# Kernel tuning notes

Hardware: AMD Instinct MI355X
Metric: run time of the kernel (lower is better)

The kernel has to match this reference:

```python
import jax, jax.numpy as jnp
import numpy as np

EPS = 1e-5
NEG_SLOPE = 0.2

def _bn(h, gamma, beta, axes):
    # training-mode batch norm (batch statistics), matching torch BN forward in train mode
    mu = jnp.mean(h, axis=axes, keepdims=True)
    var = jnp.var(h, axis=axes, keepdims=True)
    return (h - mu) * jax.lax.rsqrt(var + EPS) * gamma + beta

def _lrelu(h):
    return jnp.where(h >= 0, h, NEG_SLOPE * h)

def _edge_conv(x, idx, W, gamma, beta):
    # x: (B,N,C) channels-last; idx: (B,N,k) neighbor indices into N
    # gathered[b,n,j,c] = x[b, idx[b,n,j], c]
    gathered = jnp.take_along_axis(x[:, None, :, :], idx[:, :, :, None], axis=2)  # (B,N,k,C)
    xc = jnp.broadcast_to(x[:, :, None, :], gathered.shape)
    feat = jnp.concatenate([gathered - xc, xc], axis=-1)          # (B,N,k,2C)
    h = jnp.einsum('bnkc,oc->bnko', feat, W)                       # 1x1 conv
    h = _lrelu(_bn(h, gamma, beta, axes=(0, 1, 2)))
    return jnp.max(h, axis=2)                                      # max over k -> (B,N,O)

def setup_inputs() -> dict:
    key = jax.random.key(0)
    ks = jax.random.split(key, 20)
    B, N, K = 8, 2048, 20
    d = {
        'x': jax.random.normal(ks[0], (B, 3, N), jnp.float32),
        'geod_dist': jax.random.normal(ks[1], (B, N, N), jnp.float32),
        'W1': jax.random.normal(ks[2], (64, 6), jnp.float32) * 0.1,
        'g1': jnp.ones((64,)), 'bt1': jnp.zeros((64,)),
        'W2': jax.random.normal(ks[3], (64, 128), jnp.float32) * 0.1,
        'g2': jnp.ones((64,)), 'bt2': jnp.zeros((64,)),
        'W3': jax.random.normal(ks[4], (128, 128), jnp.float32) * 0.1,
        'g3': jnp.ones((128,)), 'bt3': jnp.zeros((128,)),
        'W4': jax.random.normal(ks[5], (256, 256), jnp.float32) * 0.1,
        'g4': jnp.ones((256,)), 'bt4': jnp.zeros((256,)),
        'W5': jax.random.normal(ks[6], (1024, 512), jnp.float32) * 0.05,
        'g5': jnp.ones((1024,)), 'bt5': jnp.zeros((1024,)),
        'L1': jax.random.normal(ks[7], (512, 2048), jnp.float32) * 0.02,
        'g6': jnp.ones((512,)), 'bt6': jnp.zeros((512,)),
        'L2': jax.random.normal(ks[8], (256, 512), jnp.float32) * 0.05,
        'bl2': jnp.zeros((256,)),
        'g7': jnp.ones((256,)), 'bt7': jnp.zeros((256,)),
        'L3': jax.random.normal(ks[9], (40, 256), jnp.float32) * 0.05,
        'bl3': jnp.zeros((40,)),
    }
    return d

def reference(x, geod_dist, W1, g1, bt1, W2, g2, bt2, W3, g3, bt3, W4, g4, bt4,
              W5, g5, bt5, L1, g6, bt6, L2, bl2, g7, bt7, L3, bl3):
    K = 20
    # neighbor indices from geodesic distance (topk largest, as in source)
    idx = jax.lax.top_k(geod_dist, K)[1]            # (B,N,K)
    xt = jnp.transpose(x, (0, 2, 1))                # (B,N,3)
    x1 = _edge_conv(xt, idx, W1, g1, bt1)           # (B,N,64)
    x2 = _edge_conv(x1, idx, W2, g2, bt2)           # (B,N,64)
    x3 = _edge_conv(x2, idx, W3, g3, bt3)           # (B,N,128)
    x4 = _edge_conv(x3, idx, W4, g4, bt4)           # (B,N,256)
    cat = jnp.concatenate([x1, x2, x3, x4], axis=-1)  # (B,N,512)
    h = jnp.einsum('bnc,oc->bno', cat, W5)            # 1x1 conv1d -> (B,N,1024)
    h = _lrelu(_bn(h, g5, bt5, axes=(0, 1)))
    hmax = jnp.max(h, axis=1)                        # (B,1024)
    havg = jnp.mean(h, axis=1)                       # (B,1024)
    z = jnp.concatenate([hmax, havg], axis=1)        # (B,2048)
    z = _lrelu(_bn(z @ L1.T, g6, bt6, axes=(0,)))    # (B,512)
    z = _lrelu(_bn(z @ L2.T + bl2, g7, bt7, axes=(0,)))  # (B,256); dropout = identity (eval)
    return z @ L3.T + bl3                            # (B,40)
```

## Files before the change

### kernel.cpp

```cpp
#include <hip/hip_runtime.h>
#include <hip/hip_bf16.h>
#include <cstdint>
#include <cstddef>

#define NB 8
#define NP 2048
#define NK 20
#define BN 16384

typedef _Float16 half8 __attribute__((ext_vector_type(8)));
typedef _Float16 half4v __attribute__((ext_vector_type(4)));
typedef float f32x4 __attribute__((ext_vector_type(4)));

__device__ __forceinline__ void gload_lds16(const void* g, void* l) {
  __builtin_amdgcn_global_load_lds(
      (const __attribute__((address_space(1))) unsigned int*)g,
      (__attribute__((address_space(3))) unsigned int*)l, 16, 0, 0);
}

static constexpr size_t OFF_IDX   = 0;
static constexpr size_t OFF_XT    = OFF_IDX + (size_t)BN*NK*4;
static constexpr size_t OFF_XCATH = OFF_XT + (size_t)BN*3*4;
static constexpr size_t OFF_WT1   = OFF_XCATH + (size_t)BN*512*2;
static constexpr size_t OFF_WD1   = OFF_WT1 + 3*64*4;
static constexpr size_t OFF_BC2   = OFF_WD1 + 3*64*4;
static constexpr size_t OFF_BC3   = OFF_BC2 + (size_t)64*128*2;
static constexpr size_t OFF_BC4   = OFF_BC3 + (size_t)64*256*2;
static constexpr size_t OFF_B5    = OFF_BC4 + (size_t)128*512*2;
static constexpr size_t OFF_YH    = OFF_B5 + (size_t)512*1024*2;
static constexpr size_t OFF_HMAX  = OFF_YH + (size_t)BN*512*2;
static constexpr size_t OFF_HMIN  = OFF_HMAX + (size_t)BN*256*4;
static constexpr size_t OFF_H5    = OFF_HMAX;
static constexpr size_t OFF_PART  = OFF_HMIN + (size_t)BN*256*4;
static constexpr size_t OFF_PMEAN = OFF_PART + (size_t)8*1024*1024;
static constexpr size_t OFF_SS    = OFF_PMEAN + (size_t)8*8*1024*4;
static constexpr size_t OFF_Z     = OFF_SS + 2*1024*4;
static constexpr size_t OFF_Z1P   = OFF_Z + (size_t)NB*2048*4;
static constexpr size_t OFF_Z1    = OFF_Z1P + NB*512*4;
static constexpr size_t OFF_Z2P   = OFF_Z1 + NB*512*4;
static constexpr size_t OFF_Z2    = OFF_Z2P + NB*256*4;

__device__ __forceinline__ void prep_b_dev(const float* __restrict__ W,
                                           _Float16* __restrict__ Bp, int t,
                                           int K2, int lgO, int lgRS) {
  int O = 1 << lgO;
  int o = t & (O - 1), k = t >> lgO;
  float v = W[((size_t)o << lgRS) + k];
  int ch = k >> 6, ks = (k >> 5) & 1, kg = (k >> 3) & 3, e = k & 7;
  int sl = o >> 4, ol = o & 15;
  size_t flat = (((size_t)(ch * 2 + ks) * (O >> 4) + sl) * 64 + (kg * 16 + ol)) * 8 + e;
  Bp[flat] = (_Float16)v;
}

__device__ __forceinline__ void prep_bc_dev(const float* __restrict__ W,
                                            _Float16* __restrict__ Bp, int t,
                                            int C, int lgO2, int lgRS) {
  int O2 = 1 << lgO2, O = O2 >> 1;
  int o2 = t & (O2 - 1), k = t >> lgO2;
  float v;
  if (o2 < O) v = W[((size_t)o2 << lgRS) + k];
  else {
    int o = o2 - O;
    v = W[((size_t)o << lgRS) + C + k] - W[((size_t)o << lgRS) + k];
  }
  int ch = k >> 6, ks = (k >> 5) & 1, kg = (k >> 3) & 3, e = k & 7;
  int sl = o2 >> 4, ol = o2 & 15;
  size_t flat = (((size_t)(ch * 2 + ks) * (O2 >> 4) + sl) * 64 + (kg * 16 + ol)) * 8 + e;
  Bp[flat] = (_Float16)v;
}

static constexpr int PB_TR  = 0;
static constexpr int PB_W1  = PB_TR + 192;
static constexpr int PB_BC2 = PB_W1 + 1;
static constexpr int PB_BC3 = PB_BC2 + 32;
static constexpr int PB_BC4 = PB_BC3 + 64;
static constexpr int PB_B5  = PB_BC4 + 256;
static constexpr int PB_END = PB_B5 + 2048;

__global__ __launch_bounds__(256) void k_prep_all(
    const float* __restrict__ x, float* __restrict__ xt,
    const float* __restrict__ W1, float* __restrict__ wt1, float* __restrict__ wd1,
    const float* __restrict__ W2, _Float16* __restrict__ bc2,
    const float* __restrict__ W3, _Float16* __restrict__ bc3,
    const float* __restrict__ W4, _Float16* __restrict__ bc4,
    const float* __restrict__ W5, _Float16* __restrict__ b5) {
  int blk = blockIdx.x, tid = threadIdx.x;
  if (blk < PB_W1) {
    int t = blk * 256 + tid;
    int n = t & (NP - 1);
    int c = (t / NP) % 3;
    int b = t / (3 * NP);
    xt[(size_t)(b * NP + n) * 3 + c] = x[t];
  } else if (blk < PB_BC2) {
    int t = tid;
    if (t < 192) {
      int o = t & 63, c = t >> 6;
      float w0 = W1[o * 6 + c];
      float w1 = W1[o * 6 + 3 + c];
      wt1[c * 64 + o] = w0;
      wd1[c * 64 + o] = w1 - w0;
    }
  } else if (blk < PB_BC3) prep_bc_dev(W2, bc2, (blk - PB_BC2) * 256 + tid, 64, 7, 7);
  else if (blk < PB_BC4)   prep_bc_dev(W3, bc3, (blk - PB_BC3) * 256 + tid, 64, 8, 7);
  else if (blk < PB_B5)    prep_bc_dev(W4, bc4, (blk - PB_BC4) * 256 + tid, 128, 9, 8);
  else                     prep_b_dev(W5, b5,   (blk - PB_B5) * 256 + tid, 512, 10, 9);
}

template <int CTRL>
__device__ __forceinline__ float dppmax(float x) {
  int t = __builtin_amdgcn_update_dpp(__float_as_int(x), __float_as_int(x),
                                      CTRL, 0xF, 0xF, false);
  return fmaxf(x, __int_as_float(t));
}
template <int CTRL>
__device__ __forceinline__ int dppmin(int x) {
  int t = __builtin_amdgcn_update_dpp(x, x, CTRL, 0xF, 0xF, false);
  return (t < x) ? t : x;
}
__device__ __forceinline__ float wave_max63(float x) {
  x = dppmax<0x111>(x); x = dppmax<0x112>(x); x = dppmax<0x114>(x);
  x = dppmax<0x118>(x); x = dppmax<0x142>(x); x = dppmax<0x143>(x);
  return x;
}
__device__ __forceinline__ int wave_min63(int x) {
  x = dppmin<0x111>(x); x = dppmin<0x112>(x); x = dppmin<0x114>(x);
  x = dppmin<0x118>(x); x = dppmin<0x142>(x); x = dppmin<0x143>(x);
  return x;
}

#define INS3(val, gi, m1, i1, m2, i2, m3, i3)            \
  {                                                      \
    bool c1 = (val) > m1;                                \
    float t_ = c1 ? m1 : (val); int ti_ = c1 ? i1 : (gi);\
    m1 = c1 ? (val) : m1;       i1 = c1 ? (gi) : i1;     \
    bool c2 = t_ > m2;                                   \
    float t2_ = c2 ? m2 : t_;   int t2i_ = c2 ? i2 : ti_;\
    m2 = c2 ? t_ : m2;          i2 = c2 ? ti_ : i2;      \
    bool c3 = t2_ > m3;                                  \
    m3 = c3 ? t2_ : m3;         i3 = c3 ? t2i_ : i3;     \
  }

#define SCAN3(v, m1, i1, m2, i2, m3, i3)                               \
  _Pragma("unroll")                                                    \
  for (int r = 0; r < 8; ++r) {                                        \
    float vals[4] = {v[r].x, v[r].y, v[r].z, v[r].w};                  \
    _Pragma("unroll")                                                  \
    for (int e = 0; e < 4; ++e) {                                      \
      float val = vals[e];                                             \
      int gi = r * 256 + l * 4 + e;                                    \
      INS3(val, gi, m1, i1, m2, i2, m3, i3)                            \
    }                                                                  \
  }

#define SCAN3M(v, dead, m1, i1, m2, i2, m3, i3)                        \
  _Pragma("unroll")                                                    \
  for (int r = 0; r < 8; ++r) {                                        \
    float vals[4] = {v[r].x, v[r].y, v[r].z, v[r].w};                  \
    _Pragma("unroll")                                                  \
    for (int e = 0; e < 4; ++e) {                                      \
      int el = r * 4 + e;                                              \
      float val = ((dead >> el) & 1u) ? NEG : vals[e];                 \
      int gi = r * 256 + l * 4 + e;                                    \
      INS3(val, gi, m1, i1, m2, i2, m3, i3)                            \
    }                                                                  \
  }

__global__ __launch_bounds__(256) void k_topk(const float* __restrict__ geod,
                                              int* __restrict__ idx) {
  int wv = threadIdx.x >> 6, l = threadIdx.x & 63;
  int row = blockIdx.x * 4 + wv;
  const float* g = geod + (size_t)row * NP;
  float4 v[8];
#pragma unroll
  for (int r = 0; r < 8; ++r) v[r] = *(const float4*)&g[r * 256 + l * 4];
  const float NEG = -__builtin_huge_valf();
  unsigned int dead = 0;
  float m1 = NEG, m2 = NEG, m3 = NEG;
  int i1 = 0, i2 = 0, i3 = 0;
  SCAN3(v, m1, i1, m2, i2, m3, i3)
  for (int it = 0; it < NK; ++it) {
    float xr = wave_max63(m1);
    float cv = __int_as_float(__builtin_amdgcn_readlane(__float_as_int(xr), 63));
    int ci = (m1 == cv) ? i1 : (1 << 30);
    ci = wave_min63(ci);
    int best_i = __builtin_amdgcn_readlane(ci, 63);
    if (l == 0) idx[(size_t)row * NK + it] = best_i;
    if (((best_i >> 2) & 63) == l) {
      dead |= 1u << (((best_i >> 8) << 2) | (best_i & 3));
      m1 = m2; i1 = i2; m2 = m3; i2 = i3; m3 = NEG; i3 = 0;
      if (m1 == NEG) { SCAN3M(v, dead, m1, i1, m2, i2, m3, i3) }
    }
  }
}

__global__ __launch_bounds__(256) void k_edge1(
    const float* __restrict__ xt, const int* __restrict__ idx,
    const float* __restrict__ wt1, const float* __restrict__ wd1,
    float* __restrict__ hmax, float* __restrict__ hmin,
    float* __restrict__ part) {
  __shared__ float xl[NP * 3];
  __shared__ int lidx[32 * NK];
  __shared__ float red[256];
  int tid = threadIdx.x;
  int b = blockIdx.x >> 6;
  int grp = blockIdx.x & 63;
  int p0 = grp * 32;
  for (int u = tid; u < NP * 3; u += 256) xl[u] = xt[(size_t)b * NP * 3 + u];
  for (int u = tid; u < 32 * NK; u += 256) lidx[u] = idx[((size_t)b * NP + p0) * NK + u];
  __syncthreads();
  int o = tid & 63;
  int pb = tid >> 6;
  float w0 = wt1[o], w1 = wt1[64 + o], w2 = wt1[128 + o];
  float d0 = wd1[o], d1 = wd1[64 + o], d2 = wd1[128 + o];
  float ps = 0.f, ps2 = 0.f;
#pragma unroll
  for (int i = 0; i < 8; ++i) {
    int pp = pb * 8 + i;
    int p = p0 + pp;
    float base = xl[p * 3] * d0 + xl[p * 3 + 1] * d1 + xl[p * 3 + 2] * d2;
    float mx = -3.4e38f, mn = 3.4e38f;
    for (int j = 0; j < NK; ++j) {
      int nb = lidx[pp * NK + j];
      float h = base + xl[nb * 3] * w0 + xl[nb * 3 + 1] * w1 + xl[nb * 3 + 2] * w2;
      mx = fmaxf(mx, h); mn = fminf(mn, h);
      ps += h; ps2 += h * h;
    }
    size_t P = (size_t)b * NP + p;
    hmax[P * 64 + o] = mx;
    hmin[P * 64 + o] = mn;
  }
  red[tid] = ps;
  __syncthreads();
  if (tid < 64) {
    float a = red[tid] + red[64 + tid] + red[128 + tid] + red[192 + tid];
    part[(size_t)blockIdx.x * 64 + tid] = a;
  }
  __syncthreads();
  red[tid] = ps2;
  __syncthreads();
  if (tid < 64) {
    float a = red[tid] + red[64 + tid] + red[128 + tid] + red[192 + tid];
    part[((size_t)gridDim.x + blockIdx.x) * 64 + tid] = a;
  }
}

template <int C, int O2, int NSPLIT>
__global__ __launch_bounds__(256) void k_dense_mfma(
    const _Float16* __restrict__ xh, int in_off,
    const _Float16* __restrict__ Bp, _Float16* __restrict__ yH) {
  constexpr int NCH = C / 64;
  constexpr int NO = O2 / NSPLIT;
  constexpr int NSLO = NO / 16;
  constexpr int NS = NSLO / 2;
  constexpr int PAIRS = 2 * NSLO;
  __shared__ __align__(16) _Float16 ldsA[64 * 64];
  __shared__ __align__(16) _Float16 ldsB[PAIRS * 512];
  int tid = threadIdx.x, wv = tid >> 6, l = tid & 63;
  int mblk = blockIdx.x, nid = 0;
  if (NSPLIT > 1) { nid = mblk >> 8; mblk &= 255; }
  int m0 = mblk * 64;
  int n_base = nid * NO;
  int mg = wv & 1, ng = wv >> 1;
  f32x4 acc[2][NS];
#pragma unroll
  for (int m = 0; m < 2; ++m)
#pragma unroll
    for (int s = 0; s < NS; ++s)
#pragma unroll
      for (int r = 0; r < 4; ++r) acc[m][s][r] = 0.f;

  for (int ch = 0; ch < NCH; ++ch) {
#pragma unroll
    for (int it = 0; it < 2; ++it) {
      int r0 = wv * 16 + it * 8;
      int R = r0 + (l >> 3);
      int q = (l & 7) ^ (l >> 3);
      gload_lds16(xh + (size_t)(m0 + R) * 512 + in_off + ch * 64 + q * 8, ldsA + r0 * 64);
    }
    for (int u = wv; u < PAIRS; u += 4) {
      int ks = u / NSLO, sloc = u - ks * NSLO;
      gload_lds16(Bp + ((size_t)((ch * 2 + ks) * (O2 / 16) + (n_base >> 4) + sloc) * 64 + l) * 8,
                  ldsB + u * 512);
    }
    __syncthreads();
#pragma unroll
    for (int ks = 0; ks < 2; ++ks) {
      half8 b[NS];
#pragma unroll
      for (int s = 0; s < NS; ++s)
        b[s] = *(const half8*)(ldsB + (ks * NSLO + ng * NS + s) * 512 + l * 8);
#pragma unroll
      for (int mt = 0; mt < 2; ++mt) {
        int row = mg * 32 + mt * 16 + (l & 15);
        int slot = (ks * 4 + (l >> 4)) ^ (row & 7);
        half8 a = *(const half8*)(ldsA + row * 64 + slot * 8);
#pragma unroll
        for (int s = 0; s < NS; ++s)
          acc[mt][s] = __builtin_amdgcn_mfma_f32_16x16x32_f16(a, b[s], acc[mt][s], 0, 0, 0);
      }
    }
    __syncthreads();
  }
  int g = l >> 4;
#pragma unroll
  for (int s = 0; s < NS; ++s) {
    int col = n_base + ng * (NS * 16) + s * 16 + (l & 15);
#pragma unroll
    for (int mt = 0; mt < 2; ++mt)
#pragma unroll
      for (int r = 0; r < 4; ++r) {
        int row = m0 + mg * 32 + mt * 16 + 4 * g + r;
        yH[(size_t)row * O2 + col] = (_Float16)acc[mt][s][r];
      }
  }
}

template <int O>
__global__ __launch_bounds__(256) void k_gather(
    const _Float16* __restrict__ yH, const int* __restrict__ idx,
    float* __restrict__ hmax, float* __restrict__ hmin,
    float* __restrict__ part) {
  constexpr int O2 = 2 * O;
  constexpr int CG = O / 4;
  constexpr int PPB = 256 / CG;
  __shared__ int lidx[PPB * NK];
  __shared__ float4 redS[256], redQ[256];
  int tid = threadIdx.x;
  int p0 = blockIdx.x * PPB;
  int bbase = p0 & ~(NP - 1);
  for (int u = tid; u < PPB * NK; u += 256) lidx[u] = idx[(size_t)p0 * NK + u];
  __syncthreads();
  int pp = tid / CG, g = tid - pp * CG;
  int p = p0 + pp;
  half4v sb4 = *(const half4v*)&yH[(size_t)p * O2 + O + g * 4];
  float sb[4] = {(float)sb4[0], (float)sb4[1], (float)sb4[2], (float)sb4[3]};
  float mx[4], mn[4], sm[4], sq[4];
#pragma unroll
  for (int e = 0; e < 4; ++e) { mx[e] = -3.4e38f; mn[e] = 3.4e38f; sm[e] = 0.f; sq[e] = 0.f; }
#pragma unroll
  for (int j = 0; j < NK; ++j) {
    int nb = bbase + lidx[pp * NK + j];
    half4v y4 = *(const half4v*)&yH[(size_t)nb * O2 + g * 4];
#pragma unroll
    for (int e = 0; e < 4; ++e) {
      float h = (float)y4[e] + sb[e];
      mx[e] = fmaxf(mx[e], h); mn[e] = fminf(mn[e], h);
      sm[e] += h; sq[e] += h * h;
    }
  }
  *(float4*)&hmax[(size_t)p * O + g * 4] = make_float4(mx[0], mx[1], mx[2], mx[3]);
  *(float4*)&hmin[(size_t)p * O + g * 4] = make_float4(mn[0], mn[1], mn[2], mn[3]);
  redS[tid] = make_float4(sm[0], sm[1], sm[2], sm[3]);
  redQ[tid] = make_float4(sq[0], sq[1], sq[2], sq[3]);
  __syncthreads();
  if (tid < CG) {
    float4 a = redS[tid], q = redQ[tid];
    for (int k = 1; k < PPB; ++k) {
      float4 b = redS[tid + k * CG], c = redQ[tid + k * CG];
      a.x += b.x; a.y += b.y; a.z += b.z; a.w += b.w;
      q.x += c.x; q.y += c.y; q.z += c.z; q.w += c.w;
    }
    *(float4*)&part[(size_t)blockIdx.x * O + tid * 4] = a;
    *(float4*)&part[((size_t)gridDim.x + blockIdx.x) * O + tid * 4] = q;
  }
}

__global__ __launch_bounds__(256) void k_conv5_mfma(
    const _Float16* __restrict__ xh, const _Float16* __restrict__ Bp,
    _Float16* __restrict__ h5, float* __restrict__ part) {
  __shared__ __align__(16) _Float16 ldsA[64 * 64];
  __shared__ __align__(16) _Float16 ldsB[32 * 512];
  __shared__ float ldsS[2][256], ldsQ[2][256], ldsMx[2][256], ldsMn[2][256];
  int tid = threadIdx.x, wv = tid >> 6, l = tid & 63;
  int mblk = blockIdx.x & 255, nid = blockIdx.x >> 8;
  int m0 = mblk * 64;
  int n_base = nid * 256;
  int mg = wv & 1, ng = wv >> 1;
  f32x4 acc[2][8];
#pragma unroll
  for (int m = 0; m < 2; ++m)
#pragma unroll
    for (int s = 0; s < 8; ++s)
#pragma unroll
      for (int r = 0; r < 4; ++r) acc[m][s][r] = 0.f;

  for (int ch = 0; ch < 8; ++ch) {
#pragma unroll
    for (int it = 0; it < 2; ++it) {
      int r0 = wv * 16 + it * 8;
      int R = r0 + (l >> 3);
      int q = (l & 7) ^ (l >> 3);
      gload_lds16(xh + (size_t)(m0 + R) * 512 + ch * 64 + q * 8, ldsA + r0 * 64);
    }
    for (int u = wv; u < 32; u += 4) {
      int ks = u >> 4, sloc = u & 15;
      gload_lds16(Bp + ((size_t)((ch * 2 + ks) * 64 + (n_base >> 4) + sloc) * 64 + l) * 8,
                  ldsB + u * 512);
    }
    __syncthreads();
#pragma unroll
    for (int ks = 0; ks < 2; ++ks) {
      half8 b[8];
#pragma unroll
      for (int s = 0; s < 8; ++s)
        b[s] = *(const half8*)(ldsB + (ks * 16 + ng * 8 + s) * 512 + l * 8);
#pragma unroll
      for (int mt = 0; mt < 2; ++mt) {
        int row = mg * 32 + mt * 16 + (l & 15);
        int slot = (ks * 4 + (l >> 4)) ^ (row & 7);
        half8 a = *(const half8*)(ldsA + row * 64 + slot * 8);
#pragma unroll
        for (int s = 0; s < 8; ++s)
          acc[mt][s] = __builtin_amdgcn_mfma_f32_16x16x32_f16(a, b[s], acc[mt][s], 0, 0, 0);
      }
    }
    __syncthreads();
  }
  int g = l >> 4;
#pragma unroll
  for (int s = 0; s < 8; ++s) {
    float sm = 0.f, sq = 0.f, mx = -3.4e38f, mn = 3.4e38f;
    int col = n_base + ng * 128 + s * 16 + (l & 15);
#pragma unroll
    for (int mt = 0; mt < 2; ++mt)
#pragma unroll
      for (int r = 0; r < 4; ++r) {
        float v = acc[mt][s][r];
        int row = m0 + mg * 32 + mt * 16 + 4 * g + r;
        h5[(size_t)row * 1024 + col] = (_Float16)v;
        sm += v; sq += v * v; mx = fmaxf(mx, v); mn = fminf(mn, v);
      }
    sm += __shfl_xor(sm, 16); sm += __shfl_xor(sm, 32);
    sq += __shfl_xor(sq, 16); sq += __shfl_xor(sq, 32);
    mx = fmaxf(mx, __shfl_xor(mx, 16)); mx = fmaxf(mx, __shfl_xor(mx, 32));
    mn = fminf(mn, __shfl_xor(mn, 16)); mn = fminf(mn, __shfl_xor(mn, 32));
    if (l < 16) {
      int u = ng * 128 + s * 16 + l;
      ldsS[mg][u] = sm; ldsQ[mg][u] = sq; ldsMx[mg][u] = mx; ldsMn[mg][u] = mn;
    }
  }
  __syncthreads();
  {
    int u = tid;
    int col = n_base + u;
    part[(size_t)mblk * 1024 + col] = ldsS[0][u] + ldsS[1][u];
    part[((size_t)256 + mblk) * 1024 + col] = ldsQ[0][u] + ldsQ[1][u];
    part[((size_t)512 + mblk) * 1024 + col] = fmaxf(ldsMx[0][u], ldsMx[1][u]);
    part[((size_t)768 + mblk) * 1024 + col] = fminf(ldsMn[0][u], ldsMn[1][u]);
  }
}

__global__ __launch_bounds__(256) void k_finalize(
    const float* __restrict__ part, int G, int O, float inv_count,
    const float* __restrict__ gamma, const float* __restrict__ beta,
    float* __restrict__ ss) {
  int o = blockIdx.x;
  float s = 0.f, s2 = 0.f;
  for (int g = threadIdx.x; g < G; g += 256) {
    s  += part[(size_t)g * O + o];
    s2 += part[((size_t)G + g) * O + o];
  }
#pragma unroll
  for (int sft = 32; sft; sft >>= 1) {
    s  += __shfl_down(s, sft);
    s2 += __shfl_down(s2, sft);
  }
  __shared__ float aw[4], aw2[4];
  int w = threadIdx.x >> 6;
  if ((threadIdx.x & 63) == 0) { aw[w] = s; aw2[w] = s2; }
  __syncthreads();
  if (threadIdx.x == 0) {
    s = aw[0] + aw[1] + aw[2] + aw[3];
    s2 = aw2[0] + aw2[1] + aw2[2] + aw2[3];
    float m   = s * inv_count;
    float var = s2 * inv_count - m * m;
    float scale = gamma[o] * rsqrtf(var + 1e-5f);
    ss[o]     = scale;
    ss[O + o] = beta[o] - m * scale;
  }
}

__global__ void k_edge_apply(const float* __restrict__ hmax, const float* __restrict__ hmin,
                             const float* __restrict__ ss, _Float16* __restrict__ xh,
                             int O, int off) {
  int t = blockIdx.x * 256 + threadIdx.x;
  int o = t % O;
  int p = t / O;
  float scale = ss[o], shift = ss[O + o];
  float v = (scale >= 0.f) ? hmax[t] : hmin[t];
  v = scale * v + shift;
  v = (v >= 0.f) ? v : 0.2f * v;
  xh[(size_t)p * 512 + off + o] = (_Float16)v;
}

__global__ __launch_bounds__(256) void k_pool5a(const _Float16* __restrict__ h5,
                                                const float* __restrict__ ss,
                                                float* __restrict__ pmean) {
  int bi = blockIdx.x;
  int b = bi >> 5, ns = (bi >> 2) & 7, cg = bi & 3;
  int col = cg * 256 + threadIdx.x;
  float scale = ss[col], shift = ss[1024 + col];
  float sm = 0.f;
  for (int n = ns * 256; n < ns * 256 + 256; ++n) {
    float v = (float)h5[(size_t)(b * 2048 + n) * 1024 + col];
    float y = scale * v + shift;
    y = (y >= 0.f) ? y : 0.2f * y;
    sm += y;
  }
  pmean[(size_t)(b * 8 + ns) * 1024 + col] = sm;
}

__global__ __launch_bounds__(256) void k_pool5b(const float* __restrict__ part,
                                                const float* __restrict__ pmean,
                                                const float* __restrict__ ss,
                                                float* __restrict__ z) {
  int bi = blockIdx.x;
  int b = bi >> 2, cg = bi & 3;
  int col = cg * 256 + threadIdx.x;
  float scale = ss[col], shift = ss[1024 + col];
  const float* pmx = part + (size_t)512 * 1024;
  const float* pmn = part + (size_t)768 * 1024;
  float mxh = -3.4e38f, mnh = 3.4e38f;
  for (int q = 0; q < 32; ++q) {
    size_t base = (size_t)(b * 32 + q) * 1024 + col;
    mxh = fmaxf(mxh, pmx[base]);
    mnh = fminf(mnh, pmn[base]);
  }
  float hsel = (scale >= 0.f) ? mxh : mnh;
  float zmax = scale * hsel + shift;
  zmax = (zmax >= 0.f) ? zmax : 0.2f * zmax;
  float sm = 0.f;
  for (int ns = 0; ns < 8; ++ns) sm += pmean[(size_t)(b * 8 + ns) * 1024 + col];
  z[b * 2048 + col] = zmax;
  z[b * 2048 + 1024 + col] = sm * (1.f / 2048.f);
}

__global__ __launch_bounds__(64) void k_fc(const float* __restrict__ in,
                                           const float* __restrict__ Wf,
                                           const float* __restrict__ bias,
                                           float* __restrict__ out, int IN, int O) {
  int blk = blockIdx.x;
  int b = blk / O, o = blk % O;
  const float4* a = (const float4*)(in + (size_t)b * IN);
  const float4* w = (const float4*)(Wf + (size_t)o * IN);
  float s = 0.f;
  for (int i = threadIdx.x; i < (IN >> 2); i += 64) {
    float4 av = a[i], wv = w[i];
    s += av.x * wv.x + av.y * wv.y + av.z * wv.z + av.w * wv.w;
  }
#pragma unroll
  for (int sft = 32; sft; sft >>= 1) s += __shfl_down(s, sft);
  if (threadIdx.x == 0) out[(size_t)b * O + o] = s + (bias ? bias[o] : 0.f);
}

__global__ void k_bn_fc(const float* __restrict__ pre, const float* __restrict__ gamma,
                        const float* __restrict__ beta, float* __restrict__ out, int O) {
  int o = blockIdx.x * 256 + threadIdx.x;
  if (o >= O) return;
  float v[NB];
  float s = 0.f, s2 = 0.f;
#pragma unroll
  for (int b = 0; b < NB; ++b) {
    v[b] = pre[(size_t)b * O + o];
    s += v[b]; s2 += v[b] * v[b];
  }
  float m = s * (1.f / NB);
  float var = s2 * (1.f / NB) - m * m;
  float scale = gamma[o] * rsqrtf(var + 1e-5f);
  float shift = beta[o] - m * scale;
#pragma unroll
  for (int b = 0; b < NB; ++b) {
    float x = scale * v[b] + shift;
    out[(size_t)b * O + o] = (x >= 0.f) ? x : 0.2f * x;
  }
}

extern "C" void kernel_launch(void* const* d_in, const int* in_sizes, int n_in,
                              void* d_out, int out_size, void* d_ws, size_t ws_size,
                              hipStream_t stream) {
  (void)in_sizes; (void)n_in; (void)out_size; (void)ws_size;
  const float* x    = (const float*)d_in[0];
  const float* geod = (const float*)d_in[1];
  const float* W1   = (const float*)d_in[2];
  const float* g1   = (const float*)d_in[3];
  const float* bt1  = (const float*)d_in[4];
  const float* W2   = (const float*)d_in[5];
  const float* g2   = (const float*)d_in[6];
  const float* bt2  = (const float*)d_in[7];
  const float* W3   = (const float*)d_in[8];
  const float* g3   = (const float*)d_in[9];
  const float* bt3  = (const float*)d_in[10];
  const float* W4   = (const float*)d_in[11];
  const float* g4   = (const float*)d_in[12];
  const float* bt4  = (const float*)d_in[13];
  const float* W5   = (const float*)d_in[14];
  const float* g5   = (const float*)d_in[15];
  const float* bt5  = (const float*)d_in[16];
  const float* L1   = (const float*)d_in[17];
  const float* g6   = (const float*)d_in[18];
  const float* bt6  = (const float*)d_in[19];
  const float* L2   = (const float*)d_in[20];
  const float* bl2  = (const float*)d_in[21];
  const float* g7   = (const float*)d_in[22];
  const float* bt7  = (const float*)d_in[23];
  const float* L3   = (const float*)d_in[24];
  const float* bl3  = (const float*)d_in[25];

  char* ws = (char*)d_ws;
  int*       idx   = (int*)(ws + OFF_IDX);
  float*     xt    = (float*)(ws + OFF_XT);
  _Float16*  xcatH = (_Float16*)(ws + OFF_XCATH);
  float*     wt1   = (float*)(ws + OFF_WT1);
  float*     wd1   = (float*)(ws + OFF_WD1);
  _Float16*  bc2   = (_Float16*)(ws + OFF_BC2);
  _Float16*  bc3   = (_Float16*)(ws + OFF_BC3);
  _Float16*  bc4   = (_Float16*)(ws + OFF_BC4);
  _Float16*  b5    = (_Float16*)(ws + OFF_B5);
  _Float16*  yH    = (_Float16*)(ws + OFF_YH);
  float*     hmax  = (float*)(ws + OFF_HMAX);
  float*     hmin  = (float*)(ws + OFF_HMIN);
  _Float16*  h5    = (_Float16*)(ws + OFF_H5);
  float*     part  = (float*)(ws + OFF_PART);
  float*     pmean = (float*)(ws + OFF_PMEAN);
  float*     ssb   = (float*)(ws + OFF_SS);
  float*     z     = (float*)(ws + OFF_Z);
  float*     z1p   = (float*)(ws + OFF_Z1P);
  float*     z1    = (float*)(ws + OFF_Z1);
  float*     z2p   = (float*)(ws + OFF_Z2P);
  float*     z2    = (float*)(ws + OFF_Z2);

  const float invE = 1.f / (float)(BN * NK);
  const float inv5 = 1.f / (float)(BN);

  k_prep_all<<<PB_END, 256, 0, stream>>>(x, xt, W1, wt1, wd1,
                                         W2, bc2, W3, bc3, W4, bc4, W5, b5);
  k_topk<<<BN / 4, 256, 0, stream>>>(geod, idx);

  k_edge1<<<512, 256, 0, stream>>>(xt, idx, wt1, wd1, hmax, hmin, part);
  k_finalize<<<64, 256, 0, stream>>>(part, 512, 64, invE, g1, bt1, ssb);
  k_edge_apply<<<(BN * 64) / 256, 256, 0, stream>>>(hmax, hmin, ssb, xcatH, 64, 0);
  k_dense_mfma<64, 128, 1><<<256, 256, 0, stream>>>(xcatH, 0, bc2, yH);
  k_gather<64><<<BN / 16, 256, 0, stream>>>(yH, idx, hmax, hmin, part);
  k_finalize<<<64, 256, 0, stream>>>(part, BN / 16, 64, invE, g2, bt2, ssb);
  k_edge_apply<<<(BN * 64) / 256, 256, 0, stream>>>(hmax, hmin, ssb, xcatH, 64, 64);
  k_dense_mfma<64, 256, 1><<<256, 256, 0, stream>>>(xcatH, 64, bc3, yH);
  k_gather<128><<<BN / 8, 256, 0, stream>>>(yH, idx, hmax, hmin, part);
  k_finalize<<<128, 256, 0, stream>>>(part, BN / 8, 128, invE, g3, bt3, ssb);
  k_edge_apply<<<(BN * 128) / 256, 256, 0, stream>>>(hmax, hmin, ssb, xcatH, 128, 128);
  k_dense_mfma<128, 512, 2><<<512, 256, 0, stream>>>(xcatH, 128, bc4, yH);
  k_gather<256><<<BN / 4, 256, 0, stream>>>(yH, idx, hmax, hmin, part);
  k_finalize<<<256, 256, 0, stream>>>(part, BN / 4, 256, invE, g4, bt4, ssb);
  k_edge_apply<<<(BN * 256) / 256, 256, 0, stream>>>(hmax, hmin, ssb, xcatH, 256, 256);

  k_conv5_mfma<<<1024, 256, 0, stream>>>(xcatH, b5, h5, part);
  k_finalize<<<1024, 256, 0, stream>>>(part, 256, 1024, inv5, g5, bt5, ssb);
  k_pool5a<<<256, 256, 0, stream>>>(h5, ssb, pmean);
  k_pool5b<<<32, 256, 0, stream>>>(part, pmean, ssb, z);

  k_fc<<<NB * 512, 64, 0, stream>>>(z, L1, nullptr, z1p, 2048, 512);
  k_bn_fc<<<2, 256, 0, stream>>>(z1p, g6, bt6, z1, 512);
  k_fc<<<NB * 256, 64, 0, stream>>>(z1, L2, bl2, z2p, 512, 256);
  k_bn_fc<<<1, 256, 0, stream>>>(z2p, g7, bt7, z2, 256);
  k_fc<<<NB * 40, 64, 0, stream>>>(z2, L3, bl3, (float*)d_out, 256, 40);
}
```

Measured before the change: 243.3 us.

## Store only gamma-selected max/min, pack topk argmax, vectorise apply, fuse FC head

Edge-conv gather kernels now write a single per-channel extreme (max or min, chosen by the sign of gamma) instead of both max and min arrays, halving that write and read traffic; conv5 partials likewise keep only the selected extreme. Top-k maps floats to order-preserving unsigned keys and does a single packed (value, index) DPP reduction per step instead of a max reduction followed by an index min reduction. The edge apply kernel processes four channels per thread with vector loads and stores. The tail FC/BN layers after L1 are fused into one single-block kernel, removing several small launches.

```diff
diff --git a/kernel.cpp b/kernel.cpp
--- a/kernel.cpp
+++ b/kernel.cpp
@@ -28,17 +28,14 @@
 static constexpr size_t OFF_BC4   = OFF_BC3 + (size_t)64*256*2;
 static constexpr size_t OFF_B5    = OFF_BC4 + (size_t)128*512*2;
 static constexpr size_t OFF_YH    = OFF_B5 + (size_t)512*1024*2;
-static constexpr size_t OFF_HMAX  = OFF_YH + (size_t)BN*512*2;
-static constexpr size_t OFF_HMIN  = OFF_HMAX + (size_t)BN*256*4;
-static constexpr size_t OFF_H5    = OFF_HMAX;
-static constexpr size_t OFF_PART  = OFF_HMIN + (size_t)BN*256*4;
+static constexpr size_t OFF_HSEL  = OFF_YH + (size_t)BN*512*2;
+static constexpr size_t OFF_SPARE = OFF_HSEL + (size_t)BN*256*4;
+static constexpr size_t OFF_H5    = OFF_HSEL;
+static constexpr size_t OFF_PART  = OFF_SPARE + (size_t)BN*256*4;
 static constexpr size_t OFF_PMEAN = OFF_PART + (size_t)8*1024*1024;
 static constexpr size_t OFF_SS    = OFF_PMEAN + (size_t)8*8*1024*4;
 static constexpr size_t OFF_Z     = OFF_SS + 2*1024*4;
 static constexpr size_t OFF_Z1P   = OFF_Z + (size_t)NB*2048*4;
-static constexpr size_t OFF_Z1    = OFF_Z1P + NB*512*4;
-static constexpr size_t OFF_Z2P   = OFF_Z1 + NB*512*4;
-static constexpr size_t OFF_Z2    = OFF_Z2P + NB*256*4;
 
 __device__ __forceinline__ void prep_b_dev(const float* __restrict__ W,
                                            _Float16* __restrict__ Bp, int t,
@@ -106,89 +103,85 @@
   else                     prep_b_dev(W5, b5,   (blk - PB_B5) * 256 + tid, 512, 10, 9);
 }
 
-template <int CTRL>
-__device__ __forceinline__ float dppmax(float x) {
-  int t = __builtin_amdgcn_update_dpp(__float_as_int(x), __float_as_int(x),
-                                      CTRL, 0xF, 0xF, false);
-  return fmaxf(x, __int_as_float(t));
-}
-template <int CTRL>
-__device__ __forceinline__ int dppmin(int x) {
-  int t = __builtin_amdgcn_update_dpp(x, x, CTRL, 0xF, 0xF, false);
-  return (t < x) ? t : x;
-}
-__device__ __forceinline__ float wave_max63(float x) {
-  x = dppmax<0x111>(x); x = dppmax<0x112>(x); x = dppmax<0x114>(x);
-  x = dppmax<0x118>(x); x = dppmax<0x142>(x); x = dppmax<0x143>(x);
-  return x;
-}
-__device__ __forceinline__ int wave_min63(int x) {
-  x = dppmin<0x111>(x); x = dppmin<0x112>(x); x = dppmin<0x114>(x);
-  x = dppmin<0x118>(x); x = dppmin<0x142>(x); x = dppmin<0x143>(x);
-  return x;
-}
-
-#define INS3(val, gi, m1, i1, m2, i2, m3, i3)            \
+__device__ __forceinline__ unsigned fmap(float x) {
+  unsigned b = __float_as_uint(x);
+  return b ^ (unsigned)(((int)b >> 31) | 0x80000000);
+}
+
+#define INS3U(u, gi, m1, i1, m2, i2, m3, i3)             \
   {                                                      \
-    bool c1 = (val) > m1;                                \
-    float t_ = c1 ? m1 : (val); int ti_ = c1 ? i1 : (gi);\
-    m1 = c1 ? (val) : m1;       i1 = c1 ? (gi) : i1;     \
+    bool c1 = (u) > m1;                                  \
+    unsigned t_ = c1 ? m1 : (u); int ti_ = c1 ? i1 : (gi);\
+    m1 = c1 ? (u) : m1;          i1 = c1 ? (gi) : i1;    \
     bool c2 = t_ > m2;                                   \
-    float t2_ = c2 ? m2 : t_;   int t2i_ = c2 ? i2 : ti_;\
-    m2 = c2 ? t_ : m2;          i2 = c2 ? ti_ : i2;      \
+    unsigned t2_ = c2 ? m2 : t_; int t2i_ = c2 ? i2 : ti_;\
+    m2 = c2 ? t_ : m2;           i2 = c2 ? ti_ : i2;     \
     bool c3 = t2_ > m3;                                  \
-    m3 = c3 ? t2_ : m3;         i3 = c3 ? t2i_ : i3;     \
-  }
-
-#define SCAN3(v, m1, i1, m2, i2, m3, i3)                               \
+    m3 = c3 ? t2_ : m3;          i3 = c3 ? t2i_ : i3;    \
+  }
+
+#define SCAN3U(uv, m1, i1, m2, i2, m3, i3)                             \
   _Pragma("unroll")                                                    \
   for (int r = 0; r < 8; ++r) {                                        \
-    float vals[4] = {v[r].x, v[r].y, v[r].z, v[r].w};                  \
     _Pragma("unroll")                                                  \
     for (int e = 0; e < 4; ++e) {                                      \
-      float val = vals[e];                                             \
+      unsigned val = uv[r][e];                                         \
       int gi = r * 256 + l * 4 + e;                                    \
-      INS3(val, gi, m1, i1, m2, i2, m3, i3)                            \
+      INS3U(val, gi, m1, i1, m2, i2, m3, i3)                           \
     }                                                                  \
   }
 
-#define SCAN3M(v, dead, m1, i1, m2, i2, m3, i3)                        \
+#define SCAN3UM(uv, dead, m1, i1, m2, i2, m3, i3)                      \
   _Pragma("unroll")                                                    \
   for (int r = 0; r < 8; ++r) {                                        \
-    float vals[4] = {v[r].x, v[r].y, v[r].z, v[r].w};                  \
     _Pragma("unroll")                                                  \
     for (int e = 0; e < 4; ++e) {                                      \
       int el = r * 4 + e;                                              \
-      float val = ((dead >> el) & 1u) ? NEG : vals[e];                 \
+      unsigned val = ((dead >> el) & 1u) ? 0u : uv[r][e];              \
       int gi = r * 256 + l * 4 + e;                                    \
-      INS3(val, gi, m1, i1, m2, i2, m3, i3)                            \
+      INS3U(val, gi, m1, i1, m2, i2, m3, i3)                           \
     }                                                                  \
   }
+
+template <int CTRL>
+__device__ __forceinline__ void dpp_pair_max(unsigned& hi, unsigned& lo) {
+  unsigned h2 = (unsigned)__builtin_amdgcn_update_dpp((int)hi, (int)hi, CTRL, 0xF, 0xF, false);
+  unsigned l2 = (unsigned)__builtin_amdgcn_update_dpp((int)lo, (int)lo, CTRL, 0xF, 0xF, false);
+  bool take = (h2 > hi) || (h2 == hi && l2 > lo);
+  hi = take ? h2 : hi;
+  lo = take ? l2 : lo;
+}
 
 __global__ __launch_bounds__(256) void k_topk(const float* __restrict__ geod,
                                               int* __restrict__ idx) {
   int wv = threadIdx.x >> 6, l = threadIdx.x & 63;
   int row = blockIdx.x * 4 + wv;
   const float* g = geod + (size_t)row * NP;
-  float4 v[8];
-#pragma unroll
-  for (int r = 0; r < 8; ++r) v[r] = *(const float4*)&g[r * 256 + l * 4];
-  const float NEG = -__builtin_huge_valf();
+  unsigned uv[8][4];
+#pragma unroll
+  for (int r = 0; r < 8; ++r) {
+    float4 v = *(const float4*)&g[r * 256 + l * 4];
+    uv[r][0] = fmap(v.x); uv[r][1] = fmap(v.y);
+    uv[r][2] = fmap(v.z); uv[r][3] = fmap(v.w);
+  }
   unsigned int dead = 0;
-  float m1 = NEG, m2 = NEG, m3 = NEG;
+  unsigned m1 = 0, m2 = 0, m3 = 0;
   int i1 = 0, i2 = 0, i3 = 0;
-  SCAN3(v, m1, i1, m2, i2, m3, i3)
+  SCAN3U(uv, m1, i1, m2, i2, m3, i3)
   for (int it = 0; it < NK; ++it) {
-    float xr = wave_max63(m1);
-    float cv = __int_as_float(__builtin_amdgcn_readlane(__float_as_int(xr), 63));
-    int ci = (m1 == cv) ? i1 : (1 << 30);
-    ci = wave_min63(ci);
-    int best_i = __builtin_amdgcn_readlane(ci, 63);
+    unsigned hi = m1, lo = ~(unsigned)i1;
+    dpp_pair_max<0x111>(hi, lo);
+    dpp_pair_max<0x112>(hi, lo);
+    dpp_pair_max<0x114>(hi, lo);
+    dpp_pair_max<0x118>(hi, lo);
+    dpp_pair_max<0x142>(hi, lo);
+    dpp_pair_max<0x143>(hi, lo);
+    int best_i = ~(unsigned)__builtin_amdgcn_readlane((int)lo, 63);
     if (l == 0) idx[(size_t)row * NK + it] = best_i;
     if (((best_i >> 2) & 63) == l) {
       dead |= 1u << (((best_i >> 8) << 2) | (best_i & 3));
-      m1 = m2; i1 = i2; m2 = m3; i2 = i3; m3 = NEG; i3 = 0;
-      if (m1 == NEG) { SCAN3M(v, dead, m1, i1, m2, i2, m3, i3) }
+      m1 = m2; i1 = i2; m2 = m3; i2 = i3; m3 = 0; i3 = 0;
+      if (m1 == 0) { SCAN3UM(uv, dead, m1, i1, m2, i2, m3, i3) }
     }
   }
 }
@@ -196,8 +189,8 @@
 __global__ __launch_bounds__(256) void k_edge1(
     const float* __restrict__ xt, const int* __restrict__ idx,
     const float* __restrict__ wt1, const float* __restrict__ wd1,
-    float* __restrict__ hmax, float* __restrict__ hmin,
-    float* __restrict__ part) {
+    const float* __restrict__ gamma,
+    float* __restrict__ hsel, float* __restrict__ part) {
   __shared__ float xl[NP * 3];
   __shared__ int lidx[32 * NK];
   __shared__ float red[256];
@@ -212,6 +205,7 @@
   int pb = tid >> 6;
   float w0 = wt1[o], w1 = wt1[64 + o], w2 = wt1[128 + o];
   float d0 = wd1[o], d1 = wd1[64 + o], d2 = wd1[128 + o];
+  bool pos = gamma[o] >= 0.f;
   float ps = 0.f, ps2 = 0.f;
 #pragma unroll
   for (int i = 0; i < 8; ++i) {
@@ -226,8 +220,7 @@
       ps += h; ps2 += h * h;
     }
     size_t P = (size_t)b * NP + p;
-    hmax[P * 64 + o] = mx;
-    hmin[P * 64 + o] = mn;
+    hsel[P * 64 + o] = pos ? mx : mn;
   }
   red[tid] = ps;
   __syncthreads();
@@ -318,8 +311,8 @@
 template <int O>
 __global__ __launch_bounds__(256) void k_gather(
     const _Float16* __restrict__ yH, const int* __restrict__ idx,
-    float* __restrict__ hmax, float* __restrict__ hmin,
-    float* __restrict__ part) {
+    const float* __restrict__ gamma,
+    float* __restrict__ hsel, float* __restrict__ part) {
   constexpr int O2 = 2 * O;
   constexpr int CG = O / 4;
   constexpr int PPB = 256 / CG;
@@ -334,6 +327,7 @@
   int p = p0 + pp;
   half4v sb4 = *(const half4v*)&yH[(size_t)p * O2 + O + g * 4];
   float sb[4] = {(float)sb4[0], (float)sb4[1], (float)sb4[2], (float)sb4[3]};
+  float4 gv = *(const float4*)&gamma[g * 4];
   float mx[4], mn[4], sm[4], sq[4];
 #pragma unroll
   for (int e = 0; e < 4; ++e) { mx[e] = -3.4e38f; mn[e] = 3.4e38f; sm[e] = 0.f; sq[e] = 0.f; }
@@ -348,8 +342,11 @@
       sm[e] += h; sq[e] += h * h;
     }
   }
-  *(float4*)&hmax[(size_t)p * O + g * 4] = make_float4(mx[0], mx[1], mx[2], mx[3]);
-  *(float4*)&hmin[(size_t)p * O + g * 4] = make_float4(mn[0], mn[1], mn[2], mn[3]);
+  float s0 = (gv.x >= 0.f) ? mx[0] : mn[0];
+  float s1 = (gv.y >= 0.f) ? mx[1] : mn[1];
+  float s2 = (gv.z >= 0.f) ? mx[2] : mn[2];
+  float s3 = (gv.w >= 0.f) ? mx[3] : mn[3];
+  *(float4*)&hsel[(size_t)p * O + g * 4] = make_float4(s0, s1, s2, s3);
   redS[tid] = make_float4(sm[0], sm[1], sm[2], sm[3]);
   redQ[tid] = make_float4(sq[0], sq[1], sq[2], sq[3]);
   __syncthreads();
@@ -367,6 +364,7 @@
 
 __global__ __launch_bounds__(256) void k_conv5_mfma(
     const _Float16* __restrict__ xh, const _Float16* __restrict__ Bp,
+    const float* __restrict__ gamma,
     _Float16* __restrict__ h5, float* __restrict__ part) {
   __shared__ __align__(16) _Float16 ldsA[64 * 64];
   __shared__ __align__(16) _Float16 ldsB[32 * 512];
@@ -445,8 +443,9 @@
     int col = n_base + u;
     part[(size_t)mblk * 1024 + col] = ldsS[0][u] + ldsS[1][u];
     part[((size_t)256 + mblk) * 1024 + col] = ldsQ[0][u] + ldsQ[1][u];
-    part[((size_t)512 + mblk) * 1024 + col] = fmaxf(ldsMx[0][u], ldsMx[1][u]);
-    part[((size_t)768 + mblk) * 1024 + col] = fminf(ldsMn[0][u], ldsMn[1][u]);
+    float sel = (gamma[col] >= 0.f) ? fmaxf(ldsMx[0][u], ldsMx[1][u])
+                                    : fminf(ldsMn[0][u], ldsMn[1][u]);
+    part[((size_t)512 + mblk) * 1024 + col] = sel;
   }
 }
 
@@ -480,17 +479,25 @@
   }
 }
 
-__global__ void k_edge_apply(const float* __restrict__ hmax, const float* __restrict__ hmin,
+__global__ void k_edge_apply(const float* __restrict__ hsel,
                              const float* __restrict__ ss, _Float16* __restrict__ xh,
                              int O, int off) {
   int t = blockIdx.x * 256 + threadIdx.x;
-  int o = t % O;
-  int p = t / O;
-  float scale = ss[o], shift = ss[O + o];
-  float v = (scale >= 0.f) ? hmax[t] : hmin[t];
-  v = scale * v + shift;
-  v = (v >= 0.f) ? v : 0.2f * v;
-  xh[(size_t)p * 512 + off + o] = (_Float16)v;
+  int cgn = O >> 2;
+  int gq = t % cgn;
+  int p = t / cgn;
+  int o = gq * 4;
+  float4 sc = *(const float4*)&ss[o];
+  float4 sh = *(const float4*)&ss[O + o];
+  float4 v = *(const float4*)&hsel[(size_t)p * O + o];
+  float y0 = sc.x * v.x + sh.x; y0 = (y0 >= 0.f) ? y0 : 0.2f * y0;
+  float y1 = sc.y * v.y + sh.y; y1 = (y1 >= 0.f) ? y1 : 0.2f * y1;
+  float y2 = sc.z * v.z + sh.z; y2 = (y2 >= 0.f) ? y2 : 0.2f * y2;
+  float y3 = sc.w * v.w + sh.w; y3 = (y3 >= 0.f) ? y3 : 0.2f * y3;
+  half4v out;
+  out[0] = (_Float16)y0; out[1] = (_Float16)y1;
+  out[2] = (_Float16)y2; out[3] = (_Float16)y3;
+  *(half4v*)&xh[(size_t)p * 512 + off + o] = out;
 }
 
 __global__ __launch_bounds__(256) void k_pool5a(const _Float16* __restrict__ h5,
@@ -518,16 +525,14 @@
   int b = bi >> 2, cg = bi & 3;
   int col = cg * 256 + threadIdx.x;
   float scale = ss[col], shift = ss[1024 + col];
-  const float* pmx = part + (size_t)512 * 1024;
-  const float* pmn = part + (size_t)768 * 1024;
-  float mxh = -3.4e38f, mnh = 3.4e38f;
+  const float* psel = part + (size_t)512 * 1024;
+  bool pos = scale >= 0.f;
+  float hv = pos ? -3.4e38f : 3.4e38f;
   for (int q = 0; q < 32; ++q) {
-    size_t base = (size_t)(b * 32 + q) * 1024 + col;
-    mxh = fmaxf(mxh, pmx[base]);
-    mnh = fminf(mnh, pmn[base]);
-  }
-  float hsel = (scale >= 0.f) ? mxh : mnh;
-  float zmax = scale * hsel + shift;
+    float v = psel[(size_t)(b * 32 + q) * 1024 + col];
+    hv = pos ? fmaxf(hv, v) : fminf(hv, v);
+  }
+  float zmax = scale * hv + shift;
   zmax = (zmax >= 0.f) ? zmax : 0.2f * zmax;
   float sm = 0.f;
   for (int ns = 0; ns < 8; ++ns) sm += pmean[(size_t)(b * 8 + ns) * 1024 + col];
@@ -537,7 +542,6 @@
 
 __global__ __launch_bounds__(64) void k_fc(const float* __restrict__ in,
                                            const float* __restrict__ Wf,
-                                           const float* __restrict__ bias,
                                            float* __restrict__ out, int IN, int O) {
   int blk = blockIdx.x;
   int b = blk / O, o = blk % O;
@@ -550,28 +554,88 @@
   }
 #pragma unroll
   for (int sft = 32; sft; sft >>= 1) s += __shfl_down(s, sft);
-  if (threadIdx.x == 0) out[(size_t)b * O + o] = s + (bias ? bias[o] : 0.f);
-}
-
-__global__ void k_bn_fc(const float* __restrict__ pre, const float* __restrict__ gamma,
-                        const float* __restrict__ beta, float* __restrict__ out, int O) {
-  int o = blockIdx.x * 256 + threadIdx.x;
-  if (o >= O) return;
-  float v[NB];
-  float s = 0.f, s2 = 0.f;
-#pragma unroll
-  for (int b = 0; b < NB; ++b) {
-    v[b] = pre[(size_t)b * O + o];
-    s += v[b]; s2 += v[b] * v[b];
-  }
-  float m = s * (1.f / NB);
-  float var = s2 * (1.f / NB) - m * m;
-  float scale = gamma[o] * rsqrtf(var + 1e-5f);
-  float shift = beta[o] - m * scale;
-#pragma unroll
-  for (int b = 0; b < NB; ++b) {
-    float x = scale * v[b] + shift;
-    out[(size_t)b * O + o] = (x >= 0.f) ? x : 0.2f * x;
+  if (threadIdx.x == 0) out[(size_t)b * O + o] = s;
+}
+
+__global__ __launch_bounds__(1024) void k_head(
+    const float* __restrict__ z1p,
+    const float* __restrict__ g6, const float* __restrict__ bt6,
+    const float* __restrict__ L2, const float* __restrict__ bl2,
+    const float* __restrict__ g7, const float* __restrict__ bt7,
+    const float* __restrict__ L3, const float* __restrict__ bl3,
+    float* __restrict__ out) {
+  __shared__ float z1[NB * 512];
+  __shared__ float z2[NB * 256];
+  int tid = threadIdx.x;
+  if (tid < 512) {
+    int o = tid;
+    float v[NB], s = 0.f, s2 = 0.f;
+#pragma unroll
+    for (int b = 0; b < NB; ++b) {
+      v[b] = z1p[(size_t)b * 512 + o];
+      s += v[b]; s2 += v[b] * v[b];
+    }
+    float m = s * (1.f / NB);
+    float var = s2 * (1.f / NB) - m * m;
+    float scale = g6[o] * rsqrtf(var + 1e-5f);
+    float shift = bt6[o] - m * scale;
+#pragma unroll
+    for (int b = 0; b < NB; ++b) {
+      float y = scale * v[b] + shift;
+      z1[b * 512 + o] = (y >= 0.f) ? y : 0.2f * y;
+    }
+  }
+  __syncthreads();
+  {
+    int o = tid & 255, bp = tid >> 8;
+    int b0 = bp * 2, b1 = b0 + 1;
+    const float4* w = (const float4*)(L2 + (size_t)o * 512);
+    const float4* a0 = (const float4*)&z1[b0 * 512];
+    const float4* a1 = (const float4*)&z1[b1 * 512];
+    float s0 = 0.f, s1 = 0.f;
+    for (int i = 0; i < 128; ++i) {
+      float4 wv = w[i], v0 = a0[i], v1 = a1[i];
+      s0 += v0.x * wv.x + v0.y * wv.y + v0.z * wv.z + v0.w * wv.w;
+      s1 += v1.x * wv.x + v1.y * wv.y + v1.z * wv.z + v1.w * wv.w;
+    }
+    z2[b0 * 256 + o] = s0 + bl2[o];
+    z2[b1 * 256 + o] = s1 + bl2[o];
+  }
+  __syncthreads();
+  if (tid < 256) {
+    int o = tid;
+    float v[NB], s = 0.f, s2 = 0.f;
+#pragma unroll
+    for (int b = 0; b < NB; ++b) {
+      v[b] = z2[b * 256 + o];
+      s += v[b]; s2 += v[b] * v[b];
+    }
+    float m = s * (1.f / NB);
+    float var = s2 * (1.f / NB) - m * m;
+    float scale = g7[o] * rsqrtf(var + 1e-5f);
+    float shift = bt7[o] - m * scale;
+#pragma unroll
+    for (int b = 0; b < NB; ++b) {
+      float y = scale * v[b] + shift;
+      v[b] = (y >= 0.f) ? y : 0.2f * y;
+    }
+    __syncthreads();
+#pragma unroll
+    for (int b = 0; b < NB; ++b) z2[b * 256 + o] = v[b];
+  } else {
+    __syncthreads();
+  }
+  __syncthreads();
+  if (tid < NB * 40) {
+    int b = tid / 40, o = tid - b * 40;
+    const float4* w = (const float4*)(L3 + (size_t)o * 256);
+    const float4* a = (const float4*)&z2[b * 256];
+    float s = 0.f;
+    for (int i = 0; i < 64; ++i) {
+      float4 wv = w[i], av = a[i];
+      s += av.x * wv.x + av.y * wv.y + av.z * wv.z + av.w * wv.w;
+    }
+    out[b * 40 + o] = s + bl3[o];
   }
 }
 
@@ -617,17 +681,13 @@
   _Float16*  bc4   = (_Float16*)(ws + OFF_BC4);
   _Float16*  b5    = (_Float16*)(ws + OFF_B5);
   _Float16*  yH    = (_Float16*)(ws + OFF_YH);
-  float*     hmax  = (float*)(ws + OFF_HMAX);
-  float*     hmin  = (float*)(ws + OFF_HMIN);
+  float*     hsel  = (float*)(ws + OFF_HSEL);
   _Float16*  h5    = (_Float16*)(ws + OFF_H5);
   float*     part  = (float*)(ws + OFF_PART);
   float*     pmean = (float*)(ws + OFF_PMEAN);
   float*     ssb   = (float*)(ws + OFF_SS);
   float*     z     = (float*)(ws + OFF_Z);
   float*     z1p   = (float*)(ws + OFF_Z1P);
-  float*     z1    = (float*)(ws + OFF_Z1);
-  float*     z2p   = (float*)(ws + OFF_Z2P);
-  float*     z2    = (float*)(ws + OFF_Z2);
 
   const float invE = 1.f / (float)(BN * NK);
   const float inv5 = 1.f / (float)(BN);
@@ -636,30 +696,28 @@
                                          W2, bc2, W3, bc3, W4, bc4, W5, b5);
   k_topk<<<BN / 4, 256, 0, stream>>>(geod, idx);
 
-  k_edge1<<<512, 256, 0, stream>>>(xt, idx, wt1, wd1, hmax, hmin, part);
+  k_edge1<<<512, 256, 0, stream>>>(xt, idx, wt1, wd1, g1, hsel, part);
   k_finalize<<<64, 256, 0, stream>>>(part, 512, 64, invE, g1, bt1, ssb);
-  k_edge_apply<<<(BN * 64) / 256, 256, 0, stream>>>(hmax, hmin, ssb, xcatH, 64, 0);
+  k_edge_apply<<<(BN * 64) / 1024, 256, 0, stream>>>(hsel, ssb, xcatH, 64, 0);
   k_dense_mfma<64, 128, 1><<<256, 256, 0, stream>>>(xcatH, 0, bc2, yH);
-  k_gather<64><<<BN / 16, 256, 0, stream>>>(yH, idx, hmax, hmin, part);
+  k_gather<64><<<BN / 16, 256, 0, stream>>>(yH, idx, g2, hsel, part);
   k_finalize<<<64, 256, 0, stream>>>(part, BN / 16, 64, invE, g2, bt2, ssb);
-  k_edge_apply<<<(BN * 64) / 256, 256, 0, stream>>>(hmax, hmin, ssb, xcatH, 64, 64);
+  k_edge_apply<<<(BN * 64) / 1024, 256, 0, stream>>>(hsel, ssb, xcatH, 64, 64);
   k_dense_mfma<64, 256, 1><<<256, 256, 0, stream>>>(xcatH, 64, bc3, yH);
-  k_gather<128><<<BN / 8, 256, 0, stream>>>(yH, idx, hmax, hmin, part);
+  k_gather<128><<<BN / 8, 256, 0, stream>>>(yH, idx, g3, hsel, part);
   k_finalize<<<128, 256, 0, stream>>>(part, BN / 8, 128, invE, g3, bt3, ssb);
-  k_edge_apply<<<(BN * 128) / 256, 256, 0, stream>>>(hmax, hmin, ssb, xcatH, 128, 128);
+  k_edge_apply<<<(BN * 128) / 1024, 256, 0, stream>>>(hsel, ssb, xcatH, 128, 128);
   k_dense_mfma<128, 512, 2><<<512, 256, 0, stream>>>(xcatH, 128, bc4, yH);
-  k_gather<256><<<BN / 4, 256, 0, stream>>>(yH, idx, hmax, hmin, part);
+  k_gather<256><<<BN / 4, 256, 0, stream>>>(yH, idx, g4, hsel, part);
   k_finalize<<<256, 256, 0, stream>>>(part, BN / 4, 256, invE, g4, bt4, ssb);
-  k_edge_apply<<<(BN * 256) / 256, 256, 0, stream>>>(hmax, hmin, ssb, xcatH, 256, 256);
-
-  k_conv5_mfma<<<1024, 256, 0, stream>>>(xcatH, b5, h5, part);
+  k_edge_apply<<<(BN * 256) / 1024, 256, 0, stream>>>(hsel, ssb, xcatH, 256, 256);
+
+  k_conv5_mfma<<<1024, 256, 0, stream>>>(xcatH, b5, g5, h5, part);
   k_finalize<<<1024, 256, 0, stream>>>(part, 256, 1024, inv5, g5, bt5, ssb);
   k_pool5a<<<256, 256, 0, stream>>>(h5, ssb, pmean);
   k_pool5b<<<32, 256, 0, stream>>>(part, pmean, ssb, z);
 
-  k_fc<<<NB * 512, 64, 0, stream>>>(z, L1, nullptr, z1p, 2048, 512);
-  k_bn_fc<<<2, 256, 0, stream>>>(z1p, g6, bt6, z1, 512);
-  k_fc<<<NB * 256, 64, 0, stream>>>(z1, L2, bl2, z2p, 512, 256);
-  k_bn_fc<<<1, 256, 0, stream>>>(z2p, g7, bt7, z2, 256);
-  k_fc<<<NB * 40, 64, 0, stream>>>(z2, L3, bl3, (float*)d_out, 256, 40);
-}
+  k_fc<<<NB * 512, 64, 0, stream>>>(z, L1, z1p, 2048, 512);
+  k_head<<<1, 1024, 0, stream>>>(z1p, g6, bt6, L2, bl2, g7, bt7, L3, bl3,
+                                 (float*)d_out);
+}
```

Result: slower. 300.0 us (+23.3%).
